# Kernel optimization log

Measured on AMD Instinct MI355X. Metric: run time of the kernel, lower is better.

The kernel has to match this reference:

```python
import jax, jax.numpy as jnp
import numpy as np

N, E = 20000, 320000
IN, HID, OUT, H = 128, 32, 1, 4
EPS = 1e-16  # PyG softmax epsilon


def _p(key, shape, scale=0.05):
    return jax.random.normal(key, shape, dtype=jnp.float32) * scale


def setup_inputs() -> dict:
    key = jax.random.key(0)
    ks = jax.random.split(key, 20)
    d = {
        "x": jax.random.normal(ks[0], (N, IN), dtype=jnp.float32),
        "edge_src": jax.random.randint(ks[1], (E,), 0, N, dtype=jnp.int32),
        "edge_dst": jax.random.randint(ks[2], (E,), 0, N, dtype=jnp.int32),
        # layer 1: TransformerConv(IN, HID, H)  ->  [N, H*HID]
        "W1q": _p(ks[3], (IN, H * HID)), "b1q": jnp.zeros((H * HID,), jnp.float32),
        "W1k": _p(ks[4], (IN, H * HID)), "b1k": jnp.zeros((H * HID,), jnp.float32),
        "W1v": _p(ks[5], (IN, H * HID)), "b1v": jnp.zeros((H * HID,), jnp.float32),
        "W1s": _p(ks[6], (IN, H * HID)), "b1s": jnp.zeros((H * HID,), jnp.float32),
        # layer 2: TransformerConv(H*HID, OUT, H) -> [N, H*OUT]
        "W2q": _p(ks[7], (H * HID, H * OUT)), "b2q": jnp.zeros((H * OUT,), jnp.float32),
        "W2k": _p(ks[8], (H * HID, H * OUT)), "b2k": jnp.zeros((H * OUT,), jnp.float32),
        "W2v": _p(ks[9], (H * HID, H * OUT)), "b2v": jnp.zeros((H * OUT,), jnp.float32),
        "W2s": _p(ks[10], (H * HID, H * OUT)), "b2s": jnp.zeros((H * OUT,), jnp.float32),
        # final nn.Linear(heads, 1)
        "Wl": _p(ks[11], (H, 1)), "bl": jnp.zeros((1,), jnp.float32),
    }
    return d


def transformer_conv(x, src, dst, Wq, bq, Wk, bk, Wv, bv, Ws, bs, heads, ch):
    n = x.shape[0]
    q = (x @ Wq + bq).reshape(n, heads, ch)
    k = (x @ Wk + bk).reshape(n, heads, ch)
    v = (x @ Wv + bv).reshape(n, heads, ch)
    qi, kj, vj = q[dst], k[src], v[src]            # [E,H,C] gathers
    score = (qi * kj).sum(-1) / jnp.sqrt(jnp.float32(ch))  # [E,H]
    m = jax.ops.segment_max(score, dst, num_segments=n)    # segment softmax by target
    e = jnp.exp(score - m[dst])
    s = jax.ops.segment_sum(e, dst, num_segments=n)
    alpha = e / (s[dst] + EPS)                              # [E,H]
    agg = jax.ops.segment_sum(alpha[:, :, None] * vj, dst, num_segments=n)  # [N,H,C]
    return agg.reshape(n, heads * ch) + x @ Ws + bs          # concat + root skip


def reference(x, edge_src, edge_dst,
              W1q, b1q, W1k, b1k, W1v, b1v, W1s, b1s,
              W2q, b2q, W2k, b2k, W2v, b2v, W2s, b2s,
              Wl, bl):
    h = transformer_conv(x, edge_src, edge_dst, W1q, b1q, W1k, b1k, W1v, b1v, W1s, b1s, H, HID)
    h = jax.nn.relu(h)  # dropout is identity in eval
    h = transformer_conv(h, edge_src, edge_dst, W2q, b2q, W2k, b2k, W2v, b2v, W2s, b2s, H, OUT)
    y = h @ Wl + bl                      # [N,1]
    return y.mean(axis=0, keepdims=True)  # [1,1]
```

## Files before the change

kernel.cpp:

```cpp
#include <hip/hip_runtime.h>
#include <math.h>

static constexpr float EPS_PYG = 1e-16f;
static constexpr float INV_SQRT32 = 0.17677669529663687f;

typedef short bf16x8 __attribute__((ext_vector_type(8)));
typedef float f32x4 __attribute__((ext_vector_type(4)));

__device__ inline unsigned short f2bf(float f) {
    union { float f; unsigned u; } x; x.f = f;
    unsigned r = x.u + 0x7FFFu + ((x.u >> 16) & 1u);
    return (unsigned short)(r >> 16);
}
__device__ inline float bf_hi(unsigned u) {
    union { unsigned u; float f; } x; x.u = u & 0xFFFF0000u; return x.f;
}
__device__ inline float bf_lo(unsigned u) {
    union { unsigned u; float f; } x; x.u = u << 16; return x.f;
}

__global__ __launch_bounds__(256) void build_prep_kernel(
    const int* __restrict__ dst, int* __restrict__ deg, int* __restrict__ slot,
    int E, int nblk_deg,
    const float4* __restrict__ X, ushort4* __restrict__ Xb, int total4,
    const float* __restrict__ Wq, const float* __restrict__ Wk,
    const float* __restrict__ Wv, const float* __restrict__ Wsk,
    unsigned short* __restrict__ Wbt)
{
    const int b = blockIdx.x;
    const int t = threadIdx.x;
    if (b < nblk_deg) {
        int e = b * 256 + t;
        if (e < E) slot[e] = atomicAdd(&deg[dst[e]], 1);
    } else if (b < nblk_deg + 4) {
        int m = b - nblk_deg;
        const float* W = (m == 0) ? Wq : (m == 1) ? Wk : (m == 2) ? Wv : Wsk;
        for (int i = t; i < 16384; i += 256) {
            int k = i >> 7, nn = i & 127;
            Wbt[m * 16384 + nn * 128 + k] = f2bf(W[i]);
        }
    } else {
        int i = (b - nblk_deg - 4) * 256 + t;
        if (i < total4) {
            float4 v = X[i];
            ushort4 o;
            o.x = f2bf(v.x); o.y = f2bf(v.y); o.z = f2bf(v.z); o.w = f2bf(v.w);
            Xb[i] = o;
        }
    }
}

__global__ __launch_bounds__(1024) void scan_kernel(const int* __restrict__ deg,
                                                    int* __restrict__ row_off, int n,
                                                    float* __restrict__ out,
                                                    const float* __restrict__ bl) {
    const int t = threadIdx.x;
    const int CH = (n + 1023) >> 10;
    const int base = t * CH;
    int vals[32];
    int sum = 0;
#pragma unroll 4
    for (int i = 0; i < CH; ++i) {
        int idx = base + i;
        int v = (idx < n) ? deg[idx] : 0;
        sum += v;
        vals[i] = sum;
    }
    const int lane = t & 63;
    const int wid = t >> 6;
    int wsum = sum;
#pragma unroll
    for (int off = 1; off < 64; off <<= 1) {
        int o = __shfl_up(wsum, off, 64);
        if (lane >= off) wsum += o;
    }
    __shared__ int wtot[16];
    if (lane == 63) wtot[wid] = wsum;
    __syncthreads();
    if (t < 64) {
        int v = (t < 16) ? wtot[t] : 0;
        int inc = v;
#pragma unroll
        for (int off = 1; off < 16; off <<= 1) {
            int o = __shfl_up(inc, off, 64);
            if (t >= off) inc += o;
        }
        if (t < 16) wtot[t] = inc - v;
    }
    __syncthreads();
    const int toff = wtot[wid] + (wsum - sum);
    if (t == 0) { row_off[0] = 0; out[0] = bl[0]; }
#pragma unroll 4
    for (int i = 0; i < CH; ++i) {
        int idx = base + i;
        if (idx < n) row_off[idx + 1] = toff + vals[i];
    }
}

__global__ void scatter_kernel(const int* __restrict__ src, const int* __restrict__ dst,
                               const int* __restrict__ row_off, const int* __restrict__ slot,
                               int* __restrict__ csr_src, int E) {
    int e = blockIdx.x * blockDim.x + threadIdx.x;
    if (e < E) csr_src[row_off[dst[e]] + slot[e]] = src[e];
}

__global__ __launch_bounds__(256) void gemm1_mfma(
    const unsigned short* __restrict__ Xb, const unsigned short* __restrict__ Wbt,
    const float* __restrict__ bq, const float* __restrict__ bk,
    const float* __restrict__ bv, const float* __restrict__ bsk,
    float* __restrict__ Q, unsigned int* __restrict__ KV,
    float* __restrict__ S, int n)
{
    const int mode = blockIdx.y;

    const int tid  = threadIdx.x;
    const int wave = tid >> 6;
    const int lane = tid & 63;
    const int m    = lane & 15;
    const int quad = lane >> 4;
    const int r0   = blockIdx.x * 64 + wave * 16;

    int arow = r0 + m;
    if (arow >= n) arow = n - 1;

    if (mode == 1) {
        const unsigned short* WK = Wbt + 16384;
        const unsigned short* WV = Wbt + 2 * 16384;
        f32x4 accK[8] = {};
        f32x4 accV[8] = {};
#pragma unroll
        for (int kc = 0; kc < 128; kc += 32) {
            bf16x8 a = *(const bf16x8*)(Xb + (size_t)arow * 128 + kc + quad * 8);
#pragma unroll
            for (int ct = 0; ct < 8; ++ct) {
                bf16x8 bk8 = *(const bf16x8*)(WK + (ct * 16 + m) * 128 + kc + quad * 8);
                accK[ct] = __builtin_amdgcn_mfma_f32_16x16x32_bf16(a, bk8, accK[ct], 0, 0, 0);
                bf16x8 bv8 = *(const bf16x8*)(WV + (ct * 16 + m) * 128 + kc + quad * 8);
                accV[ct] = __builtin_amdgcn_mfma_f32_16x16x32_bf16(a, bv8, accV[ct], 0, 0, 0);
            }
        }
#pragma unroll
        for (int ct = 0; ct < 8; ++ct) {
            const int col = ct * 16 + m;
            const float bbk = bk[col], bbv = bv[col];
#pragma unroll
            for (int r = 0; r < 4; ++r) {
                const int row = r0 + quad * 4 + r;
                if (row < n) {
                    unsigned kb = f2bf(accK[ct][r] + bbk);
                    unsigned vb = f2bf(accV[ct][r] + bbv);
                    KV[(size_t)row * 128 + col] = (kb << 16) | vb;
                }
            }
        }
    } else {
        const int mat = (mode == 0) ? 0 : 3;
        const unsigned short* W = Wbt + (size_t)mat * 16384;
        const float* bias = (mode == 0) ? bq : bsk;
        float* C = (mode == 0) ? Q : S;
        f32x4 acc[8] = {};
#pragma unroll
        for (int kc = 0; kc < 128; kc += 32) {
            bf16x8 a = *(const bf16x8*)(Xb + (size_t)arow * 128 + kc + quad * 8);
#pragma unroll
            for (int ct = 0; ct < 8; ++ct) {
                bf16x8 bfr = *(const bf16x8*)(W + (ct * 16 + m) * 128 + kc + quad * 8);
                acc[ct] = __builtin_amdgcn_mfma_f32_16x16x32_bf16(a, bfr, acc[ct], 0, 0, 0);
            }
        }
#pragma unroll
        for (int ct = 0; ct < 8; ++ct) {
            const int col = ct * 16 + m;
            const float bb = bias[col];
#pragma unroll
            for (int r = 0; r < 4; ++r) {
                const int row = r0 + quad * 4 + r;
                if (row < n) C[(size_t)row * 128 + col] = acc[ct][r] + bb;
            }
        }
    }
}

__global__ __launch_bounds__(256) void l1_agg_kernel(
    const float* __restrict__ Q, const unsigned int* __restrict__ KV,
    const float* __restrict__ S,
    const int* __restrict__ row_off, const int* __restrict__ csr_src,
    float* __restrict__ H1, int n)
{
    const int t = threadIdx.x;
    const int node = blockIdx.x * 4 + (t >> 6);
    if (node >= n) return;
    const int l    = t & 31;
    const int half = (t >> 5) & 1;
    const int cbase = ((l >> 3) << 5) + ((l & 7) << 2);

    const float4 q = *(const float4*)(Q + (size_t)node * 128 + cbase);
    const int beg = row_off[node], end = row_off[node + 1];

    float lsum = 0.f, a0 = 0.f, a1 = 0.f, a2 = 0.f, a3 = 0.f;
    int pos = beg + half;
    for (; pos + 2 < end; pos += 4) {
        int s0 = csr_src[pos];
        int s1 = csr_src[pos + 2];
        uint4 u0 = *(const uint4*)(KV + (size_t)s0 * 128 + cbase);
        uint4 u1 = *(const uint4*)(KV + (size_t)s1 * 128 + cbase);
        float p0 = q.x * bf_hi(u0.x) + q.y * bf_hi(u0.y)
                 + q.z * bf_hi(u0.z) + q.w * bf_hi(u0.w);
        float p1 = q.x * bf_hi(u1.x) + q.y * bf_hi(u1.y)
                 + q.z * bf_hi(u1.z) + q.w * bf_hi(u1.w);
        p0 += __shfl_xor(p0, 4, 8);  p1 += __shfl_xor(p1, 4, 8);
        p0 += __shfl_xor(p0, 2, 8);  p1 += __shfl_xor(p1, 2, 8);
        p0 += __shfl_xor(p0, 1, 8);  p1 += __shfl_xor(p1, 1, 8);
        float e0 = __expf(p0 * INV_SQRT32);
        float e1 = __expf(p1 * INV_SQRT32);
        lsum += e0 + e1;
        a0 += e0 * bf_lo(u0.x) + e1 * bf_lo(u1.x);
        a1 += e0 * bf_lo(u0.y) + e1 * bf_lo(u1.y);
        a2 += e0 * bf_lo(u0.z) + e1 * bf_lo(u1.z);
        a3 += e0 * bf_lo(u0.w) + e1 * bf_lo(u1.w);
    }
    if (pos < end) {
        int s0 = csr_src[pos];
        uint4 u0 = *(const uint4*)(KV + (size_t)s0 * 128 + cbase);
        float p0 = q.x * bf_hi(u0.x) + q.y * bf_hi(u0.y)
                 + q.z * bf_hi(u0.z) + q.w * bf_hi(u0.w);
        p0 += __shfl_xor(p0, 4, 8);
        p0 += __shfl_xor(p0, 2, 8);
        p0 += __shfl_xor(p0, 1, 8);
        float e0 = __expf(p0 * INV_SQRT32);
        lsum += e0;
        a0 += e0 * bf_lo(u0.x);
        a1 += e0 * bf_lo(u0.y);
        a2 += e0 * bf_lo(u0.z);
        a3 += e0 * bf_lo(u0.w);
    }
    lsum += __shfl_xor(lsum, 32, 64);
    a0   += __shfl_xor(a0,   32, 64);
    a1   += __shfl_xor(a1,   32, 64);
    a2   += __shfl_xor(a2,   32, 64);
    a3   += __shfl_xor(a3,   32, 64);
    if (half == 0) {
        const float inv = 1.0f / (lsum + EPS_PYG);
        const float4 sk = *(const float4*)(S + (size_t)node * 128 + cbase);
        float4 o;
        o.x = fmaxf(a0 * inv + sk.x, 0.f);
        o.y = fmaxf(a1 * inv + sk.y, 0.f);
        o.z = fmaxf(a2 * inv + sk.z, 0.f);
        o.w = fmaxf(a3 * inv + sk.w, 0.f);
        *(float4*)(H1 + (size_t)node * 128 + cbase) = o;
    }
}

__global__ __launch_bounds__(256) void gemm2_kernel(
    const float* __restrict__ H1,
    const float* __restrict__ Wq, const float* __restrict__ Wk,
    const float* __restrict__ Wv, const float* __restrict__ Wsk,
    const float* __restrict__ bq, const float* __restrict__ bk,
    const float* __restrict__ bv, const float* __restrict__ bsk,
    float4* __restrict__ Q2, float4* __restrict__ KV2, float4* __restrict__ S2, int n)
{
    __shared__ float Hs[64][129];
    __shared__ float Wt[128][16];
    __shared__ float bt[16];

    const int tid = threadIdx.x;
    const int r0 = blockIdx.x * 64;

    for (int i = tid; i < 2048; i += 256) {
        int row = i >> 4, col = i & 15;
        int mt = col >> 2, c = col & 3;
        const float* Wm = (mt == 0) ? Wq : (mt == 1) ? Wk : (mt == 2) ? Wv : Wsk;
        Wt[row][col] = Wm[row * 4 + c];
    }
    if (tid < 16) {
        int mt = tid >> 2;
        const float* bm = (mt == 0) ? bq : (mt == 1) ? bk : (mt == 2) ? bv : bsk;
        bt[tid] = bm[tid & 3];
    }
    for (int f = tid; f < 2048; f += 256) {
        int row = f >> 5, c4 = f & 31;
        float4 val = make_float4(0.f, 0.f, 0.f, 0.f);
        if (r0 + row < n) val = ((const float4*)H1)[(size_t)(r0 + row) * 32 + c4];
        Hs[row][c4 * 4 + 0] = val.x;
        Hs[row][c4 * 4 + 1] = val.y;
        Hs[row][c4 * 4 + 2] = val.z;
        Hs[row][c4 * 4 + 3] = val.w;
    }
    __syncthreads();

    const int nl = tid & 63;
    const int jg = tid >> 6;
    float a0 = 0.f, a1 = 0.f, a2 = 0.f, a3 = 0.f;
#pragma unroll 4
    for (int k = 0; k < 128; ++k) {
        float h = Hs[nl][k];
        a0 += h * Wt[k][jg * 4 + 0];
        a1 += h * Wt[k][jg * 4 + 1];
        a2 += h * Wt[k][jg * 4 + 2];
        a3 += h * Wt[k][jg * 4 + 3];
    }
    int node = r0 + nl;
    if (node < n) {
        float4 o = make_float4(a0 + bt[jg * 4 + 0], a1 + bt[jg * 4 + 1],
                               a2 + bt[jg * 4 + 2], a3 + bt[jg * 4 + 3]);
        if (jg == 0)      Q2[node] = o;
        else if (jg == 1) KV2[(size_t)node * 2 + 0] = o;
        else if (jg == 2) KV2[(size_t)node * 2 + 1] = o;
        else              S2[node] = o;
    }
}

__global__ __launch_bounds__(256) void l2_agg_kernel(
    const float4* __restrict__ Q2, const float4* __restrict__ KV2,
    const float4* __restrict__ S2,
    const int* __restrict__ row_off, const int* __restrict__ csr_src,
    const float* __restrict__ Wl, float* __restrict__ out, int n, float invn)
{
    const int t  = threadIdx.x;
    const int g  = t >> 4;
    const int gl = t & 15;
    const int nd = blockIdx.x * 16 + g;
    float y = 0.f;
    if (nd < n) {
        const int beg = row_off[nd], end = row_off[nd + 1];
        float4 q = Q2[nd];
        float l0 = 0.f, l1 = 0.f, l2 = 0.f, l3 = 0.f;
        float a0 = 0.f, a1 = 0.f, a2 = 0.f, a3 = 0.f;
        for (int pos = beg + gl; pos < end; pos += 16) {
            int src = csr_src[pos];
            float4 k = KV2[(size_t)src * 2 + 0];
            float4 v = KV2[(size_t)src * 2 + 1];
            float e0 = __expf(q.x * k.x);
            float e1 = __expf(q.y * k.y);
            float e2 = __expf(q.z * k.z);
            float e3 = __expf(q.w * k.w);
            l0 += e0; a0 += e0 * v.x;
            l1 += e1; a1 += e1 * v.y;
            l2 += e2; a2 += e2 * v.z;
            l3 += e3; a3 += e3 * v.w;
        }
#pragma unroll
        for (int mk = 8; mk >= 1; mk >>= 1) {
            l0 += __shfl_xor(l0, mk, 16); l1 += __shfl_xor(l1, mk, 16);
            l2 += __shfl_xor(l2, mk, 16); l3 += __shfl_xor(l3, mk, 16);
            a0 += __shfl_xor(a0, mk, 16); a1 += __shfl_xor(a1, mk, 16);
            a2 += __shfl_xor(a2, mk, 16); a3 += __shfl_xor(a3, mk, 16);
        }
        if (gl == 0) {
            float4 sk = S2[nd];
            float h0 = a0 / (l0 + EPS_PYG) + sk.x;
            float h1 = a1 / (l1 + EPS_PYG) + sk.y;
            float h2 = a2 / (l2 + EPS_PYG) + sk.z;
            float h3 = a3 / (l3 + EPS_PYG) + sk.w;
            y = (h0 * Wl[0] + h1 * Wl[1] + h2 * Wl[2] + h3 * Wl[3]) * invn;
        }
    }
    __shared__ float red[256];
    red[t] = y;
    __syncthreads();
    for (int off = 128; off > 0; off >>= 1) {
        if (t < (unsigned)off) red[t] += red[t + off];
        __syncthreads();
    }
    if (t == 0) atomicAdd(out, red[0]);
}

extern "C" void kernel_launch(void* const* d_in, const int* in_sizes, int n_in,
                              void* d_out, int out_size, void* d_ws, size_t ws_size,
                              hipStream_t stream) {
    const float* x        = (const float*)d_in[0];
    const int*   edge_src = (const int*)d_in[1];
    const int*   edge_dst = (const int*)d_in[2];
    const float* W1q = (const float*)d_in[3];  const float* b1q = (const float*)d_in[4];
    const float* W1k = (const float*)d_in[5];  const float* b1k = (const float*)d_in[6];
    const float* W1v = (const float*)d_in[7];  const float* b1v = (const float*)d_in[8];
    const float* W1s = (const float*)d_in[9];  const float* b1s = (const float*)d_in[10];
    const float* W2q = (const float*)d_in[11]; const float* b2q = (const float*)d_in[12];
    const float* W2k = (const float*)d_in[13]; const float* b2k = (const float*)d_in[14];
    const float* W2v = (const float*)d_in[15]; const float* b2v = (const float*)d_in[16];
    const float* W2s = (const float*)d_in[17]; const float* b2s = (const float*)d_in[18];
    const float* Wl  = (const float*)d_in[19]; const float* bl  = (const float*)d_in[20];

    const int N = in_sizes[0] / 128;
    const int E = in_sizes[1];
    float* out = (float*)d_out;

    float* ws  = (float*)d_ws;
    size_t off = 0;
    float*        Q1  = ws + off; off += (size_t)N * 128;
    unsigned int* KV  = (unsigned int*)(ws + off); off += (size_t)N * 128;
    float*        S1  = ws + off; off += (size_t)N * 128;
    float*        H1  = ws + off; off += (size_t)N * 128;
    float*        q2  = ws + off; off += (size_t)N * 4;
    float*        kv2 = ws + off; off += (size_t)N * 8;
    float*        s2  = ws + off; off += (size_t)N * 4;
    unsigned short* Xb  = (unsigned short*)(ws + off); off += (size_t)N * 64;
    unsigned short* Wbt = (unsigned short*)(ws + off); off += 4 * 16384 / 2;
    int* ibase   = (int*)(ws + off);
    int* deg     = ibase;
    int* row_off = ibase + N;
    int* slot    = ibase + 2 * N + 4;
    int* csr_src = slot + E;

    const int nblk_e = (E + 255) / 256;
    const int total4 = N * 32;
    const int nblk_x = (total4 + 255) / 256;
    const int nblk_g = (N + 63) / 64;

    hipMemsetAsync(deg, 0, (size_t)N * sizeof(int), stream);
    build_prep_kernel<<<nblk_e + 4 + nblk_x, 256, 0, stream>>>(
        edge_dst, deg, slot, E, nblk_e,
        (const float4*)x, (ushort4*)Xb, total4, W1q, W1k, W1v, W1s, Wbt);
    scan_kernel<<<1, 1024, 0, stream>>>(deg, row_off, N, out, bl);
    scatter_kernel<<<nblk_e, 256, 0, stream>>>(edge_src, edge_dst, row_off,
                                               slot, csr_src, E);
    {
        dim3 grid(nblk_g, 3);
        gemm1_mfma<<<grid, 256, 0, stream>>>(Xb, Wbt, b1q, b1k, b1v, b1s,
                                             Q1, KV, S1, N);
    }
    l1_agg_kernel<<<(N + 3) / 4, 256, 0, stream>>>(Q1, KV, S1, row_off, csr_src, H1, N);
    gemm2_kernel<<<nblk_g, 256, 0, stream>>>(H1, W2q, W2k, W2v, W2s,
                                             b2q, b2k, b2v, b2s,
                                             (float4*)q2, (float4*)kv2,
                                             (float4*)s2, N);
    l2_agg_kernel<<<(N + 15) / 16, 256, 0, stream>>>((const float4*)q2,
                                                     (const float4*)kv2,
                                                     (const float4*)s2,
                                                     row_off, csr_src, Wl, out, N,
                                                     1.0f / (float)N);
}
```

Baseline: 237.3 us.

## Fuse layer-2 projection into layer-1 aggregation and pack Q/skip as bf16

The layer-2 GEMM kernel is removed; each node's wave now multiplies its ReLU output by the small layer-2 weights and reduces with shuffles inside the layer-1 aggregation kernel, so the H1 buffer is no longer written and re-read. The Q and skip projections are packed together as bf16 pairs, matching KV, and the GEMM grid drops to two modes each producing two outputs. The separate X-to-bf16 conversion pass is also removed; conversion now happens inline in the GEMM. This cuts launches and global traffic, but also lowers Q and skip precision to bf16 and adds shuffle reductions and redundant X conversion in each GEMM block.

```diff
diff --git a/kernel.cpp b/kernel.cpp
--- a/kernel.cpp
+++ b/kernel.cpp
@@ -22,7 +22,6 @@
 __global__ __launch_bounds__(256) void build_prep_kernel(
     const int* __restrict__ dst, int* __restrict__ deg, int* __restrict__ slot,
     int E, int nblk_deg,
-    const float4* __restrict__ X, ushort4* __restrict__ Xb, int total4,
     const float* __restrict__ Wq, const float* __restrict__ Wk,
     const float* __restrict__ Wv, const float* __restrict__ Wsk,
     unsigned short* __restrict__ Wbt)
@@ -32,20 +31,12 @@
     if (b < nblk_deg) {
         int e = b * 256 + t;
         if (e < E) slot[e] = atomicAdd(&deg[dst[e]], 1);
-    } else if (b < nblk_deg + 4) {
+    } else {
         int m = b - nblk_deg;
         const float* W = (m == 0) ? Wq : (m == 1) ? Wk : (m == 2) ? Wv : Wsk;
         for (int i = t; i < 16384; i += 256) {
             int k = i >> 7, nn = i & 127;
             Wbt[m * 16384 + nn * 128 + k] = f2bf(W[i]);
-        }
-    } else {
-        int i = (b - nblk_deg - 4) * 256 + t;
-        if (i < total4) {
-            float4 v = X[i];
-            ushort4 o;
-            o.x = f2bf(v.x); o.y = f2bf(v.y); o.z = f2bf(v.z); o.w = f2bf(v.w);
-            Xb[i] = o;
         }
     }
 }
@@ -105,11 +96,10 @@
 }
 
 __global__ __launch_bounds__(256) void gemm1_mfma(
-    const unsigned short* __restrict__ Xb, const unsigned short* __restrict__ Wbt,
+    const float* __restrict__ X, const unsigned short* __restrict__ Wbt,
     const float* __restrict__ bq, const float* __restrict__ bk,
     const float* __restrict__ bv, const float* __restrict__ bsk,
-    float* __restrict__ Q, unsigned int* __restrict__ KV,
-    float* __restrict__ S, int n)
+    unsigned int* __restrict__ QS, unsigned int* __restrict__ KV, int n)
 {
     const int mode = blockIdx.y;
 
@@ -123,78 +113,69 @@
     int arow = r0 + m;
     if (arow >= n) arow = n - 1;
 
-    if (mode == 1) {
-        const unsigned short* WK = Wbt + 16384;
-        const unsigned short* WV = Wbt + 2 * 16384;
-        f32x4 accK[8] = {};
-        f32x4 accV[8] = {};
-#pragma unroll
-        for (int kc = 0; kc < 128; kc += 32) {
-            bf16x8 a = *(const bf16x8*)(Xb + (size_t)arow * 128 + kc + quad * 8);
-#pragma unroll
-            for (int ct = 0; ct < 8; ++ct) {
-                bf16x8 bk8 = *(const bf16x8*)(WK + (ct * 16 + m) * 128 + kc + quad * 8);
-                accK[ct] = __builtin_amdgcn_mfma_f32_16x16x32_bf16(a, bk8, accK[ct], 0, 0, 0);
-                bf16x8 bv8 = *(const bf16x8*)(WV + (ct * 16 + m) * 128 + kc + quad * 8);
-                accV[ct] = __builtin_amdgcn_mfma_f32_16x16x32_bf16(a, bv8, accV[ct], 0, 0, 0);
+    const unsigned short* WA = Wbt + (size_t)(mode ? 1 : 0) * 16384;
+    const unsigned short* WB = Wbt + (size_t)(mode ? 2 : 3) * 16384;
+    const float* biasA = mode ? bk : bq;
+    const float* biasB = mode ? bv : bsk;
+    unsigned int* Out = mode ? KV : QS;
+
+    const float4* xr = (const float4*)(X + (size_t)arow * 128);
+
+    f32x4 accA[8] = {};
+    f32x4 accB[8] = {};
+#pragma unroll
+    for (int kc = 0; kc < 128; kc += 32) {
+        float4 f0 = xr[(kc >> 2) + quad * 2];
+        float4 f1 = xr[(kc >> 2) + quad * 2 + 1];
+        bf16x8 a;
+        a[0] = (short)f2bf(f0.x); a[1] = (short)f2bf(f0.y);
+        a[2] = (short)f2bf(f0.z); a[3] = (short)f2bf(f0.w);
+        a[4] = (short)f2bf(f1.x); a[5] = (short)f2bf(f1.y);
+        a[6] = (short)f2bf(f1.z); a[7] = (short)f2bf(f1.w);
+#pragma unroll
+        for (int ct = 0; ct < 8; ++ct) {
+            bf16x8 ba = *(const bf16x8*)(WA + (ct * 16 + m) * 128 + kc + quad * 8);
+            accA[ct] = __builtin_amdgcn_mfma_f32_16x16x32_bf16(a, ba, accA[ct], 0, 0, 0);
+            bf16x8 bb = *(const bf16x8*)(WB + (ct * 16 + m) * 128 + kc + quad * 8);
+            accB[ct] = __builtin_amdgcn_mfma_f32_16x16x32_bf16(a, bb, accB[ct], 0, 0, 0);
+        }
+    }
+#pragma unroll
+    for (int ct = 0; ct < 8; ++ct) {
+        const int col = ct * 16 + m;
+        const float bA = biasA[col], bB = biasB[col];
+#pragma unroll
+        for (int r = 0; r < 4; ++r) {
+            const int row = r0 + quad * 4 + r;
+            if (row < n) {
+                unsigned ha = f2bf(accA[ct][r] + bA);
+                unsigned lb = f2bf(accB[ct][r] + bB);
+                Out[(size_t)row * 128 + col] = (ha << 16) | lb;
             }
         }
-#pragma unroll
-        for (int ct = 0; ct < 8; ++ct) {
-            const int col = ct * 16 + m;
-            const float bbk = bk[col], bbv = bv[col];
-#pragma unroll
-            for (int r = 0; r < 4; ++r) {
-                const int row = r0 + quad * 4 + r;
-                if (row < n) {
-                    unsigned kb = f2bf(accK[ct][r] + bbk);
-                    unsigned vb = f2bf(accV[ct][r] + bbv);
-                    KV[(size_t)row * 128 + col] = (kb << 16) | vb;
-                }
-            }
-        }
-    } else {
-        const int mat = (mode == 0) ? 0 : 3;
-        const unsigned short* W = Wbt + (size_t)mat * 16384;
-        const float* bias = (mode == 0) ? bq : bsk;
-        float* C = (mode == 0) ? Q : S;
-        f32x4 acc[8] = {};
-#pragma unroll
-        for (int kc = 0; kc < 128; kc += 32) {
-            bf16x8 a = *(const bf16x8*)(Xb + (size_t)arow * 128 + kc + quad * 8);
-#pragma unroll
-            for (int ct = 0; ct < 8; ++ct) {
-                bf16x8 bfr = *(const bf16x8*)(W + (ct * 16 + m) * 128 + kc + quad * 8);
-                acc[ct] = __builtin_amdgcn_mfma_f32_16x16x32_bf16(a, bfr, acc[ct], 0, 0, 0);
-            }
-        }
-#pragma unroll
-        for (int ct = 0; ct < 8; ++ct) {
-            const int col = ct * 16 + m;
-            const float bb = bias[col];
-#pragma unroll
-            for (int r = 0; r < 4; ++r) {
-                const int row = r0 + quad * 4 + r;
-                if (row < n) C[(size_t)row * 128 + col] = acc[ct][r] + bb;
-            }
-        }
     }
 }
 
 __global__ __launch_bounds__(256) void l1_agg_kernel(
-    const float* __restrict__ Q, const unsigned int* __restrict__ KV,
-    const float* __restrict__ S,
+    const unsigned int* __restrict__ QS, const unsigned int* __restrict__ KV,
     const int* __restrict__ row_off, const int* __restrict__ csr_src,
-    float* __restrict__ H1, int n)
+    const float* __restrict__ W2q, const float* __restrict__ W2k,
+    const float* __restrict__ W2v, const float* __restrict__ W2s,
+    const float* __restrict__ b2q, const float* __restrict__ b2k,
+    const float* __restrict__ b2v, const float* __restrict__ b2s,
+    float4* __restrict__ Q2, float4* __restrict__ KV2, float4* __restrict__ S2,
+    int n)
 {
     const int t = threadIdx.x;
     const int node = blockIdx.x * 4 + (t >> 6);
     if (node >= n) return;
     const int l    = t & 31;
     const int half = (t >> 5) & 1;
+    const int lf   = t & 63;
     const int cbase = ((l >> 3) << 5) + ((l & 7) << 2);
 
-    const float4 q = *(const float4*)(Q + (size_t)node * 128 + cbase);
+    const uint4 qs = *(const uint4*)(QS + (size_t)node * 128 + cbase);
+    const float4 q = make_float4(bf_hi(qs.x), bf_hi(qs.y), bf_hi(qs.z), bf_hi(qs.w));
     const int beg = row_off[node], end = row_off[node + 1];
 
     float lsum = 0.f, a0 = 0.f, a1 = 0.f, a2 = 0.f, a3 = 0.f;
@@ -239,74 +220,53 @@
     a1   += __shfl_xor(a1,   32, 64);
     a2   += __shfl_xor(a2,   32, 64);
     a3   += __shfl_xor(a3,   32, 64);
-    if (half == 0) {
-        const float inv = 1.0f / (lsum + EPS_PYG);
-        const float4 sk = *(const float4*)(S + (size_t)node * 128 + cbase);
-        float4 o;
-        o.x = fmaxf(a0 * inv + sk.x, 0.f);
-        o.y = fmaxf(a1 * inv + sk.y, 0.f);
-        o.z = fmaxf(a2 * inv + sk.z, 0.f);
-        o.w = fmaxf(a3 * inv + sk.w, 0.f);
-        *(float4*)(H1 + (size_t)node * 128 + cbase) = o;
-    }
-}
-
-__global__ __launch_bounds__(256) void gemm2_kernel(
-    const float* __restrict__ H1,
-    const float* __restrict__ Wq, const float* __restrict__ Wk,
-    const float* __restrict__ Wv, const float* __restrict__ Wsk,
-    const float* __restrict__ bq, const float* __restrict__ bk,
-    const float* __restrict__ bv, const float* __restrict__ bsk,
-    float4* __restrict__ Q2, float4* __restrict__ KV2, float4* __restrict__ S2, int n)
-{
-    __shared__ float Hs[64][129];
-    __shared__ float Wt[128][16];
-    __shared__ float bt[16];
-
-    const int tid = threadIdx.x;
-    const int r0 = blockIdx.x * 64;
-
-    for (int i = tid; i < 2048; i += 256) {
-        int row = i >> 4, col = i & 15;
-        int mt = col >> 2, c = col & 3;
-        const float* Wm = (mt == 0) ? Wq : (mt == 1) ? Wk : (mt == 2) ? Wv : Wsk;
-        Wt[row][col] = Wm[row * 4 + c];
-    }
-    if (tid < 16) {
-        int mt = tid >> 2;
-        const float* bm = (mt == 0) ? bq : (mt == 1) ? bk : (mt == 2) ? bv : bsk;
-        bt[tid] = bm[tid & 3];
-    }
-    for (int f = tid; f < 2048; f += 256) {
-        int row = f >> 5, c4 = f & 31;
-        float4 val = make_float4(0.f, 0.f, 0.f, 0.f);
-        if (r0 + row < n) val = ((const float4*)H1)[(size_t)(r0 + row) * 32 + c4];
-        Hs[row][c4 * 4 + 0] = val.x;
-        Hs[row][c4 * 4 + 1] = val.y;
-        Hs[row][c4 * 4 + 2] = val.z;
-        Hs[row][c4 * 4 + 3] = val.w;
-    }
-    __syncthreads();
-
-    const int nl = tid & 63;
-    const int jg = tid >> 6;
-    float a0 = 0.f, a1 = 0.f, a2 = 0.f, a3 = 0.f;
-#pragma unroll 4
-    for (int k = 0; k < 128; ++k) {
-        float h = Hs[nl][k];
-        a0 += h * Wt[k][jg * 4 + 0];
-        a1 += h * Wt[k][jg * 4 + 1];
-        a2 += h * Wt[k][jg * 4 + 2];
-        a3 += h * Wt[k][jg * 4 + 3];
-    }
-    int node = r0 + nl;
-    if (node < n) {
-        float4 o = make_float4(a0 + bt[jg * 4 + 0], a1 + bt[jg * 4 + 1],
-                               a2 + bt[jg * 4 + 2], a3 + bt[jg * 4 + 3]);
-        if (jg == 0)      Q2[node] = o;
-        else if (jg == 1) KV2[(size_t)node * 2 + 0] = o;
-        else if (jg == 2) KV2[(size_t)node * 2 + 1] = o;
-        else              S2[node] = o;
+
+    const float inv = 1.0f / (lsum + EPS_PYG);
+    const float h0 = fmaxf(a0 * inv + bf_lo(qs.x), 0.f);
+    const float h1 = fmaxf(a1 * inv + bf_lo(qs.y), 0.f);
+    const float h2 = fmaxf(a2 * inv + bf_lo(qs.z), 0.f);
+    const float h3 = fmaxf(a3 * inv + bf_lo(qs.w), 0.f);
+
+    const float* WA = half ? W2v : W2q;
+    const float* WB = half ? W2s : W2k;
+    float p0, p1, p2, p3, p4, p5, p6, p7;
+    {
+        float4 wa = *(const float4*)(WA + (size_t)(cbase + 0) * 4);
+        float4 wb = *(const float4*)(WB + (size_t)(cbase + 0) * 4);
+        p0 = h0 * wa.x; p1 = h0 * wa.y; p2 = h0 * wa.z; p3 = h0 * wa.w;
+        p4 = h0 * wb.x; p5 = h0 * wb.y; p6 = h0 * wb.z; p7 = h0 * wb.w;
+        wa = *(const float4*)(WA + (size_t)(cbase + 1) * 4);
+        wb = *(const float4*)(WB + (size_t)(cbase + 1) * 4);
+        p0 += h1 * wa.x; p1 += h1 * wa.y; p2 += h1 * wa.z; p3 += h1 * wa.w;
+        p4 += h1 * wb.x; p5 += h1 * wb.y; p6 += h1 * wb.z; p7 += h1 * wb.w;
+        wa = *(const float4*)(WA + (size_t)(cbase + 2) * 4);
+        wb = *(const float4*)(WB + (size_t)(cbase + 2) * 4);
+        p0 += h2 * wa.x; p1 += h2 * wa.y; p2 += h2 * wa.z; p3 += h2 * wa.w;
+        p4 += h2 * wb.x; p5 += h2 * wb.y; p6 += h2 * wb.z; p7 += h2 * wb.w;
+        wa = *(const float4*)(WA + (size_t)(cbase + 3) * 4);
+        wb = *(const float4*)(WB + (size_t)(cbase + 3) * 4);
+        p0 += h3 * wa.x; p1 += h3 * wa.y; p2 += h3 * wa.z; p3 += h3 * wa.w;
+        p4 += h3 * wb.x; p5 += h3 * wb.y; p6 += h3 * wb.z; p7 += h3 * wb.w;
+    }
+#pragma unroll
+    for (int mk = 16; mk >= 1; mk >>= 1) {
+        p0 += __shfl_xor(p0, mk, 32); p1 += __shfl_xor(p1, mk, 32);
+        p2 += __shfl_xor(p2, mk, 32); p3 += __shfl_xor(p3, mk, 32);
+        p4 += __shfl_xor(p4, mk, 32); p5 += __shfl_xor(p5, mk, 32);
+        p6 += __shfl_xor(p6, mk, 32); p7 += __shfl_xor(p7, mk, 32);
+    }
+    if (lf == 0) {
+        const float4 ba = *(const float4*)b2q;
+        const float4 bb = *(const float4*)b2k;
+        Q2[node] = make_float4(p0 + ba.x, p1 + ba.y, p2 + ba.z, p3 + ba.w);
+        KV2[(size_t)node * 2 + 0] =
+            make_float4(p4 + bb.x, p5 + bb.y, p6 + bb.z, p7 + bb.w);
+    } else if (lf == 32) {
+        const float4 ba = *(const float4*)b2v;
+        const float4 bb = *(const float4*)b2s;
+        KV2[(size_t)node * 2 + 1] =
+            make_float4(p0 + ba.x, p1 + ba.y, p2 + ba.z, p3 + ba.w);
+        S2[node] = make_float4(p4 + bb.x, p5 + bb.y, p6 + bb.z, p7 + bb.w);
     }
 }
 
@@ -387,14 +347,11 @@
 
     float* ws  = (float*)d_ws;
     size_t off = 0;
-    float*        Q1  = ws + off; off += (size_t)N * 128;
+    unsigned int* QS  = (unsigned int*)(ws + off); off += (size_t)N * 128;
     unsigned int* KV  = (unsigned int*)(ws + off); off += (size_t)N * 128;
-    float*        S1  = ws + off; off += (size_t)N * 128;
-    float*        H1  = ws + off; off += (size_t)N * 128;
     float*        q2  = ws + off; off += (size_t)N * 4;
     float*        kv2 = ws + off; off += (size_t)N * 8;
     float*        s2  = ws + off; off += (size_t)N * 4;
-    unsigned short* Xb  = (unsigned short*)(ws + off); off += (size_t)N * 64;
     unsigned short* Wbt = (unsigned short*)(ws + off); off += 4 * 16384 / 2;
     int* ibase   = (int*)(ws + off);
     int* deg     = ibase;
@@ -403,27 +360,22 @@
     int* csr_src = slot + E;
 
     const int nblk_e = (E + 255) / 256;
-    const int total4 = N * 32;
-    const int nblk_x = (total4 + 255) / 256;
     const int nblk_g = (N + 63) / 64;
 
     hipMemsetAsync(deg, 0, (size_t)N * sizeof(int), stream);
-    build_prep_kernel<<<nblk_e + 4 + nblk_x, 256, 0, stream>>>(
-        edge_dst, deg, slot, E, nblk_e,
-        (const float4*)x, (ushort4*)Xb, total4, W1q, W1k, W1v, W1s, Wbt);
+    build_prep_kernel<<<nblk_e + 4, 256, 0, stream>>>(
+        edge_dst, deg, slot, E, nblk_e, W1q, W1k, W1v, W1s, Wbt);
     scan_kernel<<<1, 1024, 0, stream>>>(deg, row_off, N, out, bl);
     scatter_kernel<<<nblk_e, 256, 0, stream>>>(edge_src, edge_dst, row_off,
                                                slot, csr_src, E);
     {
-        dim3 grid(nblk_g, 3);
-        gemm1_mfma<<<grid, 256, 0, stream>>>(Xb, Wbt, b1q, b1k, b1v, b1s,
-                                             Q1, KV, S1, N);
-    }
-    l1_agg_kernel<<<(N + 3) / 4, 256, 0, stream>>>(Q1, KV, S1, row_off, csr_src, H1, N);
-    gemm2_kernel<<<nblk_g, 256, 0, stream>>>(H1, W2q, W2k, W2v, W2s,
-                                             b2q, b2k, b2v, b2s,
-                                             (float4*)q2, (float4*)kv2,
-                                             (float4*)s2, N);
+        dim3 grid(nblk_g, 2);
+        gemm1_mfma<<<grid, 256, 0, stream>>>(x, Wbt, b1q, b1k, b1v, b1s,
+                                             QS, KV, N);
+    }
+    l1_agg_kernel<<<(N + 3) / 4, 256, 0, stream>>>(
+        QS, KV, row_off, csr_src, W2q, W2k, W2v, W2s, b2q, b2k, b2v, b2s,
+        (float4*)q2, (float4*)kv2, (float4*)s2, N);
     l2_agg_kernel<<<(N + 15) / 16, 256, 0, stream>>>((const float4*)q2,
                                                      (const float4*)kv2,
                                                      (const float4*)s2,
```

Measured after the change: 232.6 us. 1.02x faster.
